# Optimization experiments

Measured on AMD Instinct MI355X. Metric: run time of the kernel, lower is better.

The kernel has to match this reference:

```python
import jax, jax.numpy as jnp
import numpy as np

B, S, Dm = 2, 4096, 1024
H, HD = 8, 128            # num_heads, head_dim
WIN, STRIDE = 512, 256    # window_size, window_size // 2
NGT = 64                  # num_global_tokens


def setup_inputs() -> dict:
    key = jax.random.key(0)
    ks = jax.random.split(key, 6)
    sc = lambda k, shape: jax.random.normal(k, shape, jnp.float32) * 0.02
    return {
        "hidden_states": jax.random.normal(ks[0], (B, S, Dm), jnp.float32),
        "global_memory": jax.random.normal(ks[1], (1, H, NGT, HD), jnp.float32),
        "conv_w": sc(ks[2], (Dm, Dm, 4)),   # (out_ch, in_ch, kernel)
        "conv_b": jnp.zeros((Dm,), jnp.float32),
        "mix_w": sc(ks[3], (2 * Dm, Dm)),
        "mix_b": jnp.zeros((Dm,), jnp.float32),
        "out_w": sc(ks[4], (Dm, Dm)),
        "out_b": jnp.zeros((Dm,), jnp.float32),
    }


def _sliding_window(x):
    nw = (S - WIN) // STRIDE + 1
    idx = np.arange(nw)[:, None] * STRIDE + np.arange(WIN)[None, :]
    w = x[:, idx, :].reshape(B, nw, WIN, H, HD)
    att = jnp.einsum('bnqhd,bnkhd->bnhqk', w, w) / np.sqrt(HD).astype(np.float32)
    att = jax.nn.softmax(att, axis=-1)
    o = jnp.einsum('bnhqk,bnkhd->bnqhd', att, w).reshape(B, nw, WIN, Dm)
    # triangular-weighted overlap-add (every window has full length here)
    tri = jnp.linspace(0.5, 1.5, WIN, dtype=x.dtype)
    contrib = (o * tri[None, None, :, None]).reshape(B, nw * WIN, Dm)
    ids = jnp.asarray(idx.reshape(-1))
    num = jax.ops.segment_sum(jnp.moveaxis(contrib, 1, 0), ids, num_segments=S)  # (S,B,Dm)
    den = jax.ops.segment_sum(jnp.tile(tri, nw), ids, num_segments=S)            # (S,)
    return jnp.moveaxis(num, 0, 1) / jnp.maximum(den, 1e-6)[None, :, None]


def _compressed_global(x, gmem, cw, cb):
    # Conv1d(k=4, stride=4) == blockwise contraction over non-overlapping groups of 4
    comp = jnp.einsum('btkd,odk->bto', x.reshape(B, S // 4, 4, Dm), cw) + cb
    comp = comp[:, :NGT].reshape(B, NGT, H, HD).transpose(0, 2, 1, 3)  # (B,H,NGT,HD)
    kv = jnp.concatenate([comp, jnp.broadcast_to(gmem, (B, H, NGT, HD))], axis=2)
    q = x.reshape(B, S, H, HD).transpose(0, 2, 1, 3)                    # (B,H,S,HD)
    att = jax.nn.softmax(jnp.einsum('bhsd,bhtd->bhst', q, kv) / np.sqrt(HD).astype(np.float32), axis=-1)
    out = jnp.einsum('bhst,bhtd->bhsd', att, kv)
    return out.transpose(0, 2, 1, 3).reshape(B, S, Dm)


def _broadcast(x):
    # exponential diffusion: O(log n) roll steps (12 for S=4096)
    result = jnp.zeros_like(x)
    cur = x
    stride = 1
    while stride < S:
        cur = cur + 0.5 * (jnp.roll(cur, stride, axis=1) + jnp.roll(cur, -stride, axis=1))
        result = result + cur
        stride *= 2
    return result / np.float32(np.log2(S) + 1.0)


def reference(hidden_states, global_memory, conv_w, conv_b, mix_w, mix_b, out_w, out_b):
    local = _sliding_window(hidden_states)
    glob = _compressed_global(hidden_states, global_memory, conv_w, conv_b)
    bc = _broadcast(hidden_states)
    gate = jax.nn.sigmoid(jnp.concatenate([local, glob], axis=-1) @ mix_w + mix_b)
    mixed = gate * local + (1.0 - gate) * glob + bc
    return mixed @ out_w + out_b
```

## Files before the change

### kernel.cpp

```cpp
#include <hip/hip_runtime.h>
#include <cstdint>

#define B_   2
#define S_   4096
#define DM   1024
#define NH   8
#define HDIM 128
#define NWIN 15

typedef __attribute__((ext_vector_type(8))) short s8v;
typedef __attribute__((ext_vector_type(4))) float f4v;

__device__ __forceinline__ float f_lo(unsigned int u){
  union { unsigned int i; float f; } v; v.i = u << 16; return v.f;
}
__device__ __forceinline__ float f_hi(unsigned int u){
  union { unsigned int i; float f; } v; v.i = u & 0xffff0000u; return v.f;
}
__device__ __forceinline__ unsigned short f2bf(float f){
  unsigned int x = __float_as_uint(f);
  x += 0x7fffu + ((x >> 16) & 1u);
  return (unsigned short)(x >> 16);
}
__device__ __forceinline__ unsigned int pack2(float a, float b){
  return (unsigned int)f2bf(a) | ((unsigned int)f2bf(b) << 16);
}

__global__ __launch_bounds__(256) void k_cvtbf(const float* __restrict__ src,
                                               unsigned short* __restrict__ dst){
  size_t i = ((size_t)blockIdx.x*256 + threadIdx.x)*8;
  float4 a = *(const float4*)(src + i);
  float4 b = *(const float4*)(src + i + 4);
  uint4 r; r.x = pack2(a.x,a.y); r.y = pack2(a.z,a.w);
  r.z = pack2(b.x,b.y); r.w = pack2(b.z,b.w);
  *(uint4*)(dst + i) = r;
}

__global__ __launch_bounds__(256) void k_xposef(const float* __restrict__ x,
                                                float* __restrict__ xT){
  __shared__ float Ls[64][68];
  const int bid = blockIdx.x;
  const int b = bid>>10, r = bid&1023, st = r>>4, dt = r&15;
  const int s0 = st*64, d0 = dt*64;
  const int tid = threadIdx.x;
#pragma unroll
  for(int p=0;p<4;p++){
    int rr = p*16 + (tid>>4), c4 = (tid&15)*4;
    *(float4*)&Ls[rr][c4] = *(const float4*)(x + ((size_t)(b*S_)+s0+rr)*DM + d0 + c4);
  }
  __syncthreads();
#pragma unroll
  for(int p=0;p<4;p++){
    int dr = p*16 + (tid>>4), c4 = (tid&15)*4;
    float4 v = { Ls[c4+0][dr], Ls[c4+1][dr], Ls[c4+2][dr], Ls[c4+3][dr] };
    *(float4*)(xT + ((size_t)(b*DM)+d0+dr)*S_ + s0 + c4) = v;
  }
}

__global__ __launch_bounds__(256) void k_diffuseT(const float* __restrict__ xT,
                                                  unsigned short* __restrict__ bcT){
  __shared__ float bufA[2][4096];
  __shared__ float bufB[2][4096];
  const int b  = blockIdx.x >> 9;
  const int d0 = (blockIdx.x & 511) * 2;
  const int tid = threadIdx.x;
  float cur[32], res[32];
#pragma unroll
  for(int k=0;k<32;k++){
    int e = tid + (k<<8); int ch = e>>12; int s = e&4095;
    float v = xT[((size_t)(b*DM)+d0+ch)*S_ + s];
    cur[k] = v; res[k] = 0.f; bufA[ch][s] = v;
  }
  __syncthreads();
#pragma unroll 1
  for(int st=0; st<12; st++){
    const int stride = 1<<st;
    float (*src)[4096] = (st&1) ? bufB : bufA;
    float (*dst)[4096] = (st&1) ? bufA : bufB;
#pragma unroll
    for(int k=0;k<32;k++){
      int e = tid + (k<<8); int ch=e>>12; int s=e&4095;
      float c = cur[k] + 0.5f*(src[ch][(s-stride)&4095] + src[ch][(s+stride)&4095]);
      dst[ch][s] = c; cur[k] = c; res[k] += c;
    }
    __syncthreads();
  }
#pragma unroll
  for(int k=0;k<32;k++){
    int e = tid + (k<<8); int ch=e>>12; int s=e&4095;
    bcT[((size_t)(b*DM)+d0+ch)*S_ + s] = f2bf(res[k]*(1.0f/13.0f));
  }
}

__global__ __launch_bounds__(256) void k_bcxpose(const unsigned short* __restrict__ bcT,
                                                 unsigned short* __restrict__ bc){
  __shared__ unsigned short Ls[64*72];
  const int bid = blockIdx.x;
  const int b = bid>>10, r = bid&1023, st = r>>4, dt = r&15;
  const int s0 = st*64, d0 = dt*64;
  const int tid = threadIdx.x;
#pragma unroll
  for(int t=0;t<2;t++){
    int cl = tid + t*256; int dr = cl>>3, c = cl&7;
    *(uint4*)&Ls[dr*72 + c*8] = *(const uint4*)(bcT + ((size_t)(b*DM)+d0+dr)*S_ + s0 + c*8);
  }
  __syncthreads();
#pragma unroll
  for(int t=0;t<2;t++){
    int cl = tid + t*256; int sr = cl>>3, c = cl&7;
    unsigned short tmp[8];
#pragma unroll
    for(int j=0;j<8;j++) tmp[j] = Ls[(c*8+j)*72 + sr];
    *(uint4*)(bc + ((size_t)(b*S_)+s0+sr)*DM + d0 + c*8) = *(const uint4*)tmp;
  }
}

__global__ __launch_bounds__(256) void k_xstage(const float* __restrict__ x,
                                                unsigned short* __restrict__ Asta){
  __shared__ float xs[4][1024];
  const int m = blockIdx.x;
  const int b = m>>6, t = m&63;
  const int tid = threadIdx.x;
  const float* xp = x + (size_t)(b*S_ + 4*t)*DM;
  for(int i=tid; i<4096; i+=256) xs[i>>10][i&1023] = xp[i];
  __syncthreads();
  float v[16];
#pragma unroll
  for(int e=0; e<16; e++) v[e] = xs[e&3][tid*4 + (e>>2)];
  uint4 r0, r1;
  r0.x = pack2(v[0],v[1]);  r0.y = pack2(v[2],v[3]);
  r0.z = pack2(v[4],v[5]);  r0.w = pack2(v[6],v[7]);
  r1.x = pack2(v[8],v[9]);  r1.y = pack2(v[10],v[11]);
  r1.z = pack2(v[12],v[13]); r1.w = pack2(v[14],v[15]);
  unsigned short* op = Asta + (size_t)m*4096 + tid*16;
  *(uint4*)op = r0;
  *(uint4*)(op+8) = r1;
}

__global__ __launch_bounds__(256) void k_gemmconv(const unsigned short* __restrict__ A,
                                                  const unsigned short* __restrict__ Bw,
                                                  float* __restrict__ part){
  __shared__ __align__(16) unsigned short As[128*64];
  __shared__ __align__(16) unsigned short Bs[128*64];
  const int nt = blockIdx.x, kt = blockIdx.y;
  const int n0 = nt<<7;
  const int tid = threadIdx.x, wid = tid>>6, lane = tid&63, quad = lane>>4, tl = lane&15;
  const int mq = (wid&1)*64, nq = (wid>>1)*64;
  f4v acc[4][4];
#pragma unroll
  for(int i=0;i<4;i++)
#pragma unroll
    for(int j=0;j<4;j++) acc[i][j] = (f4v)(0.f);

  for(int kc=kt*1024; kc<kt*1024+1024; kc+=64){
    __syncthreads();
#pragma unroll
    for(int t=0; t<4; t++){
      int cl = tid + t*256, m = cl>>3, c = cl&7;
      uint4 v = *(const uint4*)(A + (size_t)m*4096 + kc + c*8);
      *(uint4*)&As[m*64 + ((c ^ (m&7))<<3)] = v;
      uint4 w = *(const uint4*)(Bw + (size_t)(n0+m)*4096 + kc + c*8);
      *(uint4*)&Bs[m*64 + ((c ^ (m&7))<<3)] = w;
    }
    __syncthreads();
#pragma unroll
    for(int ks=0; ks<2; ks++){
      s8v af[4], bf[4];
#pragma unroll
      for(int i=0;i<4;i++){
        int ml = mq + i*16 + tl;
        af[i] = *(const s8v*)&As[ml*64 + (((ks*4+quad) ^ (ml&7))<<3)];
      }
#pragma unroll
      for(int j=0;j<4;j++){
        int nl = nq + j*16 + tl;
        bf[j] = *(const s8v*)&Bs[nl*64 + (((ks*4+quad) ^ (nl&7))<<3)];
      }
#pragma unroll
      for(int i=0;i<4;i++)
#pragma unroll
        for(int j=0;j<4;j++)
          acc[i][j] = __builtin_amdgcn_mfma_f32_16x16x32_bf16(af[i], bf[j], acc[i][j], 0, 0, 0);
    }
  }
  float* pp = part + (size_t)kt*131072;
#pragma unroll
  for(int i=0;i<4;i++)
#pragma unroll
    for(int r=0;r<4;r++){
      int m = mq + i*16 + quad*4 + r;
#pragma unroll
      for(int j=0;j<4;j++){
        int n = n0 + nq + j*16 + tl;
        pp[m*1024 + n] = acc[i][j][r];
      }
    }
}

__global__ __launch_bounds__(256) void k_convred(const float* __restrict__ part,
                                                 const float* __restrict__ cb,
                                                 unsigned short* __restrict__ kv){
  int i = blockIdx.x*256 + threadIdx.x;
  int m = i>>10, o = i&1023;
  float v = part[i] + part[131072+i] + part[262144+i] + part[393216+i] + cb[o];
  int b = m>>6, t = m&63, h = o>>7, hd = o&127;
  kv[((size_t)(b*NH + h)*128 + t)*HDIM + hd] = f2bf(v);
}

__global__ __launch_bounds__(256) void k_gmem(const float* __restrict__ g,
                                              unsigned short* __restrict__ kv){
  int i = blockIdx.x*256 + threadIdx.x;
  int hd = i & 127, gt = (i>>7)&63, h = (i>>13)&7, b = i>>16;
  kv[((size_t)(b*NH + h)*128 + 64 + gt)*HDIM + hd] = f2bf(g[((size_t)(h*64 + gt))*HDIM + hd]);
}

template<int MODE>
__global__ __launch_bounds__(256, 4) void k_attn(const unsigned short* __restrict__ xb,
                                                 const unsigned short* __restrict__ kvb,
                                                 unsigned short* __restrict__ outb){
  __shared__ __align__(16) unsigned short sh[17408];
  constexpr int KSo = 0;
  constexpr int PSo = 0;
  constexpr int VTo = 8192;

  const int b = blockIdx.y;
  int h, n, qt, nkt;
  if(MODE==0){
    int r = blockIdx.x;
    int s = (r&7)*120 + (r>>3);
    qt = s&7; h = (s>>3)&7; n = s>>6; nkt = 8;
  } else {
    int r = blockIdx.x;
    int s = (r&7)*64 + (r>>3);
    qt = s&63; h = s>>6; n = 0; nkt = 2;
  }

  const int tid  = threadIdx.x;
  const int wid  = tid>>6, lane = tid&63, quad = lane>>4, tl = lane&15;
  const int sQ   = (MODE==0) ? (n*256 + qt*64) : (qt*64);

  s8v qf[4];
  {
    int qr = sQ + wid*16 + tl;
    const unsigned short* qp = xb + ((size_t)(b*S_) + qr)*DM + h*HDIM;
#pragma unroll
    for(int ks=0; ks<4; ks++)
      qf[ks] = *(const s8v*)(qp + ks*32 + quad*8);
  }

  const unsigned short* kbase = (MODE==0)
      ? xb + ((size_t)(b*S_) + n*256)*DM + h*HDIM
      : kvb + (size_t)(b*NH+h)*128*HDIM;
  const int kstride = (MODE==0) ? DM : HDIM;
  const int mrow = (tid&15)*4;
  const int cg   = tid>>4;

  uint4 rg[4];
#pragma unroll
  for(int j=0;j<4;j++)
    rg[j] = *(const uint4*)(kbase + (size_t)(mrow+j)*kstride + cg*8);

  f4v oacc[8];
#pragma unroll
  for(int ht=0; ht<8; ht++) oacc[ht] = (f4v)(0.f);
  float l_ = 0.f;

  const float SC2 = 0.12751743f;

  for(int kt=0; kt<nkt; kt++){
    __syncthreads();
#pragma unroll
    for(int j=0;j<4;j++){
      int t = mrow + j;
      *(uint4*)&sh[KSo + t*128 + ((cg ^ (t&7))<<3)] = rg[j];
    }
    {
      const unsigned int* w0 = (const unsigned int*)&rg[0];
      const unsigned int* w1 = (const unsigned int*)&rg[1];
      const unsigned int* w2 = (const unsigned int*)&rg[2];
      const unsigned int* w3 = (const unsigned int*)&rg[3];
#pragma unroll
      for(int i=0;i<8;i++){
        int w = i>>1;
        unsigned int a, c2;
        if(i&1){ a  = (w0[w]>>16) | (w1[w] & 0xffff0000u);
                 c2 = (w2[w]>>16) | (w3[w] & 0xffff0000u); }
        else   { a  = (w0[w] & 0xffffu) | (w1[w]<<16);
                 c2 = (w2[w] & 0xffffu) | (w3[w]<<16); }
        uint2 u = {a, c2};
        *(uint2*)&sh[VTo + (cg*8+i)*72 + mrow] = u;
      }
    }
    __syncthreads();
    if(kt+1 < nkt){
      const unsigned short* np = kbase + (size_t)((kt+1)*64 + mrow)*kstride + cg*8;
#pragma unroll
      for(int j=0;j<4;j++) rg[j] = *(const uint4*)(np + (size_t)j*kstride);
    }

    f4v st[4];
    __builtin_amdgcn_s_setprio(1);
#pragma unroll
    for(int tt=0; tt<4; tt++){
      st[tt] = (f4v)(0.f);
      int row = tt*16 + tl;
#pragma unroll
      for(int ks=0; ks<4; ks++){
        s8v af = *(const s8v*)&sh[KSo + row*128 + (((ks*4+quad) ^ (row&7))<<3)];
        st[tt] = __builtin_amdgcn_mfma_f32_16x16x32_bf16(af, qf[ks], st[tt], 0, 0, 0);
      }
    }
    __builtin_amdgcn_s_setprio(0);

    {
      float ps = 0.f;
#pragma unroll
      for(int tt=0; tt<4; tt++)
#pragma unroll
        for(int r=0; r<4; r++){
          float p = exp2f(st[tt][r]*SC2);
          st[tt][r] = p; ps += p;
        }
      ps += __shfl_xor(ps, 16);
      ps += __shfl_xor(ps, 32);
      l_ += ps;
    }

    __syncthreads();

    {
      int ql = wid*16 + tl;
#pragma unroll
      for(int tt=0; tt<4; tt++){
        ushort4 u = { f2bf(st[tt][0]), f2bf(st[tt][1]),
                      f2bf(st[tt][2]), f2bf(st[tt][3]) };
        *(ushort4*)&sh[PSo + ql*64 + (((tt*2 + (quad>>1)) ^ (ql&7))<<3) + (quad&1)*4] = u;
      }
    }

    __builtin_amdgcn_s_setprio(1);
#pragma unroll
    for(int kk=0; kk<2; kk++){
      int ql = wid*16 + tl;
      s8v pb = *(const s8v*)&sh[PSo + ql*64 + (((kk*4+quad) ^ (ql&7))<<3)];
#pragma unroll
      for(int ht=0; ht<8; ht++){
        s8v vf = *(const s8v*)&sh[VTo + (ht*16 + tl)*72 + kk*32 + quad*8];
        oacc[ht] = __builtin_amdgcn_mfma_f32_16x16x32_bf16(vf, pb, oacc[ht], 0, 0, 0);
      }
    }
    __builtin_amdgcn_s_setprio(0);
  }

  {
    float inv = 1.0f/l_;
#pragma unroll
    for(int ht=0; ht<8; ht++) oacc[ht] *= inv;
  }
  __syncthreads();
  {
    int ql = wid*16 + tl;
#pragma unroll
    for(int ht=0; ht<8; ht++){
      ushort4 u = { f2bf(oacc[ht][0]), f2bf(oacc[ht][1]),
                    f2bf(oacc[ht][2]), f2bf(oacc[ht][3]) };
      *(ushort4*)&sh[ql*136 + ht*16 + quad*4] = u;
    }
  }
  __syncthreads();
  {
    int ql = tid>>2, qu = tid&3;
    size_t row = (MODE==0) ? (size_t)((b*NWIN + n)*512 + qt*64 + ql)
                           : (size_t)(b*S_ + qt*64 + ql);
    unsigned short* op = outb + row*DM + h*HDIM + qu*32;
#pragma unroll
    for(int c=0; c<4; c++){
      uint4 v = *(const uint4*)&sh[ql*136 + qu*32 + c*8];
      *(uint4*)(op + c*8) = v;
    }
  }
}

__global__ __launch_bounds__(256) void k_combine(const unsigned short* __restrict__ wso,
                                                 unsigned short* __restrict__ loc){
  const int bid = blockIdx.x;
  const int b = bid >> 12, s = bid & 4095;
  const int tid = threadIdx.x;
  const int nhi = s >> 8, sl = s & 255;
  const int c0 = tid*4;
  float n0=0.f, n1=0.f, n2=0.f, n3=0.f, den=0.f;
  if(nhi <= 14){
    float tr = 0.5f + (float)sl*(1.0f/511.0f);
    den += tr;
    uint2 u = *(const uint2*)(wso + (size_t)((b*NWIN + nhi)*512 + sl)*DM + c0);
    n0 += tr*f_lo(u.x); n1 += tr*f_hi(u.x); n2 += tr*f_lo(u.y); n3 += tr*f_hi(u.y);
  }
  if(nhi >= 1){
    int q2 = sl + 256;
    float tr = 0.5f + (float)q2*(1.0f/511.0f);
    den += tr;
    uint2 u = *(const uint2*)(wso + (size_t)((b*NWIN + nhi-1)*512 + q2)*DM + c0);
    n0 += tr*f_lo(u.x); n1 += tr*f_hi(u.x); n2 += tr*f_lo(u.y); n3 += tr*f_hi(u.y);
  }
  float di = 1.0f/den;
  uint2 o; o.x = pack2(n0*di, n1*di); o.y = pack2(n2*di, n3*di);
  *(uint2*)(loc + (size_t)(b*S_ + s)*DM + c0) = o;
}

__global__ __launch_bounds__(256) void k_wcvt(const float* __restrict__ W,
                                              unsigned short* __restrict__ WT, int K){
  __shared__ float Ls[64][68];
  int kt = blockIdx.x >> 4, nt = blockIdx.x & 15;
  int k0 = kt<<6, n0 = nt<<6;
  int tid = threadIdx.x;
#pragma unroll
  for(int p=0; p<4; p++){
    int r = p*16 + (tid>>4), c4 = (tid&15)*4;
    float4 v = *(const float4*)(W + (size_t)(k0+r)*1024 + n0 + c4);
    *(float4*)&Ls[r][c4] = v;
  }
  __syncthreads();
  int nn = tid>>2, kq = tid&3;
#pragma unroll
  for(int c=0; c<4; c++){
    int k = kq*16 + c*4;
    ushort4 u = { f2bf(Ls[k+0][nn]), f2bf(Ls[k+1][nn]), f2bf(Ls[k+2][nn]), f2bf(Ls[k+3][nn]) };
    *(ushort4*)(WT + (size_t)(n0+nn)*K + k0 + k) = u;
  }
}

template<int MODE>
__global__ __launch_bounds__(256) void k_gemm2(const unsigned short* __restrict__ A0,
                                               const unsigned short* __restrict__ A1,
                                               const unsigned short* __restrict__ WT,
                                               const float* __restrict__ bias,
                                               const unsigned short* __restrict__ loc,
                                               const unsigned short* __restrict__ glo,
                                               const unsigned short* __restrict__ bcb,
                                               unsigned short* __restrict__ outb,
                                               float* __restrict__ outf){
  const int KTOT = (MODE==0) ? 2048 : 1024;
  __shared__ __align__(16) unsigned short As[128*64];
  __shared__ __align__(16) unsigned short Bs[128*64];
  const int mt = blockIdx.x >> 3, nt = blockIdx.x & 7;
  const int m0 = mt<<7, n0 = nt<<7;
  const int tid = threadIdx.x, wid = tid>>6, lane = tid&63, quad = lane>>4, tl = lane&15;
  const int mq = (wid&1)*64, nq = (wid>>1)*64;
  f4v acc[4][4];
#pragma unroll
  for(int i=0;i<4;i++)
#pragma unroll
    for(int j=0;j<4;j++) acc[i][j] = (f4v)(0.f);

  for(int kc=0; kc<KTOT; kc+=64){
    __syncthreads();
    const unsigned short* Ab = (MODE==0 && kc>=1024) ? A1 : A0;
    const int kb = (MODE==0) ? (kc & 1023) : kc;
#pragma unroll
    for(int t=0; t<4; t++){
      int cl = tid + t*256, m = cl>>3, c = cl&7;
      uint4 v = *(const uint4*)(Ab + (size_t)(m0+m)*1024 + kb + c*8);
      *(uint4*)&As[m*64 + ((c ^ (m&7))<<3)] = v;
      uint4 w = *(const uint4*)(WT + (size_t)(n0+m)*KTOT + kc + c*8);
      *(uint4*)&Bs[m*64 + ((c ^ (m&7))<<3)] = w;
    }
    __syncthreads();
#pragma unroll
    for(int ks=0; ks<2; ks++){
      s8v af[4], bf[4];
#pragma unroll
      for(int i=0;i<4;i++){
        int ml = mq + i*16 + tl;
        af[i] = *(const s8v*)&As[ml*64 + (((ks*4+quad) ^ (ml&7))<<3)];
      }
#pragma unroll
      for(int j=0;j<4;j++){
        int nl = nq + j*16 + tl;
        bf[j] = *(const s8v*)&Bs[nl*64 + (((ks*4+quad) ^ (nl&7))<<3)];
      }
#pragma unroll
      for(int i=0;i<4;i++)
#pragma unroll
        for(int j=0;j<4;j++)
          acc[i][j] = __builtin_amdgcn_mfma_f32_16x16x32_bf16(af[i], bf[j], acc[i][j], 0, 0, 0);
    }
  }

#pragma unroll
  for(int i=0;i<4;i++){
#pragma unroll
    for(int r=0;r<4;r++){
      int m = m0 + mq + i*16 + quad*4 + r;
      size_t rowb = (size_t)m * 1024;
#pragma unroll
      for(int j=0;j<4;j++){
        int nn = n0 + nq + j*16 + tl;
        float v = acc[i][j][r] + bias[nn];
        if(MODE==0){
          float g  = 1.0f/(1.0f + __expf(-v));
          float lv = f_lo((unsigned int)loc[rowb+nn]);
          float gv = f_lo((unsigned int)glo[rowb+nn]);
          float bv = f_lo((unsigned int)bcb[rowb+nn]);
          outb[rowb+nn] = f2bf(g*lv + (1.0f-g)*gv + bv);
        } else {
          outf[rowb+nn] = v;
        }
      }
    }
  }
}

extern "C" void kernel_launch(void* const* d_in, const int* in_sizes, int n_in,
                              void* d_out, int out_size, void* d_ws, size_t ws_size,
                              hipStream_t stream){
  const float* x  = (const float*)d_in[0];
  const float* gm = (const float*)d_in[1];
  const float* cw = (const float*)d_in[2];
  const float* cb = (const float*)d_in[3];
  const float* mw = (const float*)d_in[4];
  const float* mb = (const float*)d_in[5];
  const float* ow = (const float*)d_in[6];
  const float* ob = (const float*)d_in[7];
  float* out = (float*)d_out;

  char* ws = (char*)d_ws;
  const size_t SZ = (size_t)B_*S_*DM*2;
  unsigned short* localb = (unsigned short*)(ws);
  unsigned short* globb  = (unsigned short*)(ws + SZ);
  unsigned short* bcb    = (unsigned short*)(ws + 2*SZ);
  unsigned short* kvb    = (unsigned short*)(ws + 3*SZ);
  unsigned short* wso    = (unsigned short*)(ws + 3*SZ + 524288);
  unsigned short* mixed  = wso;
  unsigned short* wt1    = (unsigned short*)(ws + 3*SZ + 524288 + SZ);
  unsigned short* wt2    = (unsigned short*)(ws + 3*SZ + 524288 + SZ + 4194304);
  unsigned short* cwb    = (unsigned short*)(ws);
  unsigned short* asta   = (unsigned short*)(ws + 8388608);
  float*          cpart  = (float*)        (ws + 9437184);
  float*          xT     = (float*)(ws + SZ);
  unsigned short* bcT    = wso;
  unsigned short* xbf    = (unsigned short*)(ws);

  k_cvtbf   <<<2048, 256, 0, stream>>>(cw, cwb);
  k_xstage  <<<128,  256, 0, stream>>>(x, asta);
  k_gemmconv<<<dim3(8,4), 256, 0, stream>>>(asta, cwb, cpart);
  k_convred <<<512,  256, 0, stream>>>(cpart, cb, kvb);
  k_gmem    <<<512,  256, 0, stream>>>(gm, kvb);
  k_xposef  <<<2048, 256, 0, stream>>>(x, xT);
  k_diffuseT<<<1024, 256, 0, stream>>>(xT, bcT);
  k_bcxpose <<<2048, 256, 0, stream>>>(bcT, bcb);
  k_cvtbf   <<<4096, 256, 0, stream>>>(x, xbf);
  k_attn<1> <<<dim3(512,2), 256, 0, stream>>>(xbf, kvb, globb);
  k_attn<0> <<<dim3(960,2), 256, 0, stream>>>(xbf, kvb, wso);
  k_combine <<<8192, 256, 0, stream>>>(wso, localb);
  k_wcvt    <<<512,  256, 0, stream>>>(mw, wt1, 2048);
  k_wcvt    <<<256,  256, 0, stream>>>(ow, wt2, 1024);
  k_gemm2<0><<<512, 256, 0, stream>>>(localb, globb, wt1, mb, localb, globb, bcb, mixed, nullptr);
  k_gemm2<1><<<512, 256, 0, stream>>>(mixed, nullptr, wt2, ob, nullptr, nullptr, nullptr, nullptr, out);
}
```

Before: 389.4 us.

## Fuse bf16 cast into transpose, register-resident diffusion tail, async LDS loads in GEMM

The fp32-to-bf16 conversion of hidden_states moves into the transpose kernel, which already reads x. This removes one full-tensor read pass and one launch. In the diffusion kernel the last four roll steps (strides 256 to 2048) now run as register shuffles within each thread, because those neighbours already sit in the same thread's registers; this drops four LDS round-trips and four barriers. The mixing and output GEMMs fill shared memory with global_load_lds direct-to-LDS loads that keep the same XOR swizzle, and they gain an occupancy hint of 3 blocks per CU, which may limit the registers available.

```diff
diff --git a/kernel.cpp b/kernel.cpp
--- a/kernel.cpp
+++ b/kernel.cpp
@@ -24,6 +24,11 @@
 }
 __device__ __forceinline__ unsigned int pack2(float a, float b){
   return (unsigned int)f2bf(a) | ((unsigned int)f2bf(b) << 16);
+}
+__device__ __forceinline__ void gl16(const unsigned short* g, unsigned short* l){
+  __builtin_amdgcn_global_load_lds(
+      (const __attribute__((address_space(1))) unsigned int*)g,
+      (__attribute__((address_space(3))) unsigned int*)l, 16, 0, 0);
 }
 
 __global__ __launch_bounds__(256) void k_cvtbf(const float* __restrict__ src,
@@ -37,7 +42,8 @@
 }
 
 __global__ __launch_bounds__(256) void k_xposef(const float* __restrict__ x,
-                                                float* __restrict__ xT){
+                                                float* __restrict__ xT,
+                                                unsigned short* __restrict__ xbf){
   __shared__ float Ls[64][68];
   const int bid = blockIdx.x;
   const int b = bid>>10, r = bid&1023, st = r>>4, dt = r&15;
@@ -46,7 +52,10 @@
 #pragma unroll
   for(int p=0;p<4;p++){
     int rr = p*16 + (tid>>4), c4 = (tid&15)*4;
-    *(float4*)&Ls[rr][c4] = *(const float4*)(x + ((size_t)(b*S_)+s0+rr)*DM + d0 + c4);
+    float4 v = *(const float4*)(x + ((size_t)(b*S_)+s0+rr)*DM + d0 + c4);
+    *(float4*)&Ls[rr][c4] = v;
+    ushort4 u = { f2bf(v.x), f2bf(v.y), f2bf(v.z), f2bf(v.w) };
+    *(ushort4*)(xbf + ((size_t)(b*S_)+s0+rr)*DM + d0 + c4) = u;
   }
   __syncthreads();
 #pragma unroll
@@ -64,26 +73,50 @@
   const int b  = blockIdx.x >> 9;
   const int d0 = (blockIdx.x & 511) * 2;
   const int tid = threadIdx.x;
-  float cur[32], res[32];
+  float curA_[32], curB_[32], res[32];
 #pragma unroll
   for(int k=0;k<32;k++){
     int e = tid + (k<<8); int ch = e>>12; int s = e&4095;
     float v = xT[((size_t)(b*DM)+d0+ch)*S_ + s];
-    cur[k] = v; res[k] = 0.f; bufA[ch][s] = v;
+    curA_[k] = v; res[k] = 0.f; bufA[ch][s] = v;
   }
   __syncthreads();
 #pragma unroll 1
-  for(int st=0; st<12; st++){
+  for(int st=0; st<8; st++){
     const int stride = 1<<st;
     float (*src)[4096] = (st&1) ? bufB : bufA;
     float (*dst)[4096] = (st&1) ? bufA : bufB;
 #pragma unroll
     for(int k=0;k<32;k++){
       int e = tid + (k<<8); int ch=e>>12; int s=e&4095;
-      float c = cur[k] + 0.5f*(src[ch][(s-stride)&4095] + src[ch][(s+stride)&4095]);
-      dst[ch][s] = c; cur[k] = c; res[k] += c;
-    }
-    __syncthreads();
+      float c = curA_[k] + 0.5f*(src[ch][(s-stride)&4095] + src[ch][(s+stride)&4095]);
+      dst[ch][s] = c; curA_[k] = c; res[k] += c;
+    }
+    __syncthreads();
+  }
+#pragma unroll
+  for(int k=0;k<32;k++){
+    int ch=k>>4, kk=k&15;
+    curB_[k] = curA_[k] + 0.5f*(curA_[ch*16 + ((kk-1)&15)] + curA_[ch*16 + ((kk+1)&15)]);
+    res[k] += curB_[k];
+  }
+#pragma unroll
+  for(int k=0;k<32;k++){
+    int ch=k>>4, kk=k&15;
+    curA_[k] = curB_[k] + 0.5f*(curB_[ch*16 + ((kk-2)&15)] + curB_[ch*16 + ((kk+2)&15)]);
+    res[k] += curA_[k];
+  }
+#pragma unroll
+  for(int k=0;k<32;k++){
+    int ch=k>>4, kk=k&15;
+    curB_[k] = curA_[k] + 0.5f*(curA_[ch*16 + ((kk-4)&15)] + curA_[ch*16 + ((kk+4)&15)]);
+    res[k] += curB_[k];
+  }
+#pragma unroll
+  for(int k=0;k<32;k++){
+    int ch=k>>4, kk=k&15;
+    curA_[k] = curB_[k] + 0.5f*(curB_[ch*16 + ((kk-8)&15)] + curB_[ch*16 + ((kk+8)&15)]);
+    res[k] += curA_[k];
   }
 #pragma unroll
   for(int k=0;k<32;k++){
@@ -430,7 +463,7 @@
 }
 
 template<int MODE>
-__global__ __launch_bounds__(256) void k_gemm2(const unsigned short* __restrict__ A0,
+__global__ __launch_bounds__(256, 3) void k_gemm2(const unsigned short* __restrict__ A0,
                                                const unsigned short* __restrict__ A1,
                                                const unsigned short* __restrict__ WT,
                                                const float* __restrict__ bias,
@@ -446,6 +479,8 @@
   const int m0 = mt<<7, n0 = nt<<7;
   const int tid = threadIdx.x, wid = tid>>6, lane = tid&63, quad = lane>>4, tl = lane&15;
   const int mq = (wid&1)*64, nq = (wid>>1)*64;
+  const int rowoff = wid*32 + (lane>>3);
+  const int cch    = (lane&7) ^ (lane>>3);
   f4v acc[4][4];
 #pragma unroll
   for(int i=0;i<4;i++)
@@ -456,13 +491,12 @@
     __syncthreads();
     const unsigned short* Ab = (MODE==0 && kc>=1024) ? A1 : A0;
     const int kb = (MODE==0) ? (kc & 1023) : kc;
-#pragma unroll
-    for(int t=0; t<4; t++){
-      int cl = tid + t*256, m = cl>>3, c = cl&7;
-      uint4 v = *(const uint4*)(Ab + (size_t)(m0+m)*1024 + kb + c*8);
-      *(uint4*)&As[m*64 + ((c ^ (m&7))<<3)] = v;
-      uint4 w = *(const uint4*)(WT + (size_t)(n0+m)*KTOT + kc + c*8);
-      *(uint4*)&Bs[m*64 + ((c ^ (m&7))<<3)] = w;
+    const unsigned short* ap = Ab + (size_t)(m0 + rowoff)*1024 + kb + cch*8;
+    const unsigned short* bp = WT + (size_t)(n0 + rowoff)*KTOT + kc + cch*8;
+#pragma unroll
+    for(int i=0;i<4;i++){
+      gl16(ap + (size_t)(i*8)*1024, &As[wid*2048 + i*512]);
+      gl16(bp + (size_t)(i*8)*KTOT, &Bs[wid*2048 + i*512]);
     }
     __syncthreads();
 #pragma unroll
@@ -545,10 +579,9 @@
   k_gemmconv<<<dim3(8,4), 256, 0, stream>>>(asta, cwb, cpart);
   k_convred <<<512,  256, 0, stream>>>(cpart, cb, kvb);
   k_gmem    <<<512,  256, 0, stream>>>(gm, kvb);
-  k_xposef  <<<2048, 256, 0, stream>>>(x, xT);
+  k_xposef  <<<2048, 256, 0, stream>>>(x, xT, xbf);
   k_diffuseT<<<1024, 256, 0, stream>>>(xT, bcT);
   k_bcxpose <<<2048, 256, 0, stream>>>(bcT, bcb);
-  k_cvtbf   <<<4096, 256, 0, stream>>>(x, xbf);
   k_attn<1> <<<dim3(512,2), 256, 0, stream>>>(xbf, kvb, globb);
   k_attn<0> <<<dim3(960,2), 256, 0, stream>>>(xbf, kvb, wso);
   k_combine <<<8192, 256, 0, stream>>>(wso, localb);
```

Result: faster. 366.1 us (-6.0%).
